# Optimization experiments

Hardware: AMD Instinct MI355X
Metric: run time of the kernel (lower is better)

The kernel has to match this reference:

```python
import jax, jax.numpy as jnp
import numpy as np

B, NE, NR, A = 512, 100000, 400, 256
ENT, REL, HIST = 200, 200, 400
ADIM = ENT + REL  # 400
HUGE = 1e31
EPS = 1e-20


def _linear(x, W, b):
    return x @ W.T + b


def setup_inputs() -> dict:
    key = jax.random.key(0)
    ks = jax.random.split(key, 26)
    w = lambda k, o, i: (jax.random.normal(k, (o, i)) * 0.02).astype(jnp.float32)
    bz = lambda o: jnp.zeros((o,), jnp.float32)
    inp = {}
    inp['H'] = jax.random.normal(ks[0], (B, HIST), jnp.float32)
    mask = (jax.random.uniform(ks[1], (B, A)) > 0.3).astype(jnp.float32)
    inp['action_mask'] = mask.at[:, 0].set(1.0)  # ensure at least one valid action
    inp['entity_emb'] = jax.random.normal(ks[2], (NE, ENT), jnp.float32) * 0.1
    inp['relation_emb'] = jax.random.normal(ks[3], (NR, REL), jnp.float32) * 0.1
    inp['W1'] = w(ks[4], ADIM, ENT + HIST + REL); inp['b1'] = bz(ADIM)
    inp['W2'] = w(ks[5], ADIM, ADIM); inp['b2'] = bz(ADIM)
    inp['W3'] = w(ks[6], REL, ENT); inp['b3'] = bz(REL)
    inp['W4'] = w(ks[7], REL, REL); inp['b4'] = bz(REL)
    inp['W5'] = w(ks[8], REL, REL + ENT); inp['b5'] = bz(REL)
    inp['W6'] = w(ks[9], REL, REL + REL); inp['b6'] = bz(REL)
    inp['Watt'] = w(ks[10], REL, ADIM + REL); inp['batt'] = bz(REL)
    inp['e'] = jax.random.randint(ks[11], (B,), 0, NE)
    inp['q'] = jax.random.randint(ks[12], (B,), 0, NR)
    inp['pred_id'] = jax.random.randint(ks[13], (B, 1), 0, NE)
    inp['r_space'] = jax.random.randint(ks[14], (B, A), 0, NR)
    inp['e_space'] = jax.random.randint(ks[15], (B, A), 0, NE)
    return inp


def reference(H, action_mask, entity_emb, relation_emb,
              W1, b1, W2, b2, W3, b3, W4, b4, W5, b5, W6, b6, Watt, batt,
              e, q, pred_id, r_space, e_space):
    # --- embed lookups ---
    Q = relation_emb[q]                 # [B, REL]
    E = entity_emb[e]                   # [B, ENT]
    # --- small MLP (dropout in eval mode -> identity) ---
    X = jax.nn.relu(_linear(jnp.concatenate([E, H, Q], -1), W1, b1))
    X2 = _linear(X, W2, b2)             # [B, ADIM]
    # --- full relation attention (multinomial sample replaced by given pred_id) ---
    pred_emb = entity_emb[pred_id]      # [B, 1, ENT]
    pred_ent_info = _linear(pred_emb, W3, b3)       # [B, 1, REL]
    relation_K = _linear(relation_emb, W4, b4)      # [NR, REL]
    local_att = jnp.einsum('bkd,rd->bkr', pred_ent_info, relation_K)  # [B,1,NR]
    beta = jnp.einsum('bkr,rd->bkd', jax.nn.softmax(local_att, -1), relation_emb).sum(1)  # [B, REL]
    # cat([R_all expand, pred_emb expand], -1).sum(1) == [sum_r R_all, NR * pred_emb]
    rel_sum = relation_emb.sum(0)                   # [REL]
    alpha_in = jnp.concatenate([jnp.broadcast_to(rel_sum, (H.shape[0], REL)),
                                NR * pred_emb[:, 0, :]], -1)
    alpha = _linear(alpha_in, W5, b5)               # [B, REL]
    V_A = _linear(jnp.concatenate([alpha, beta], -1), W6, b6)  # [B, REL]
    relation_att = jax.nn.softmax(
        _linear(jnp.concatenate([X2, V_A], -1), Watt, batt) @ relation_emb.T, -1)  # [B, NR]
    # --- policy_nn_fun: action embedding gather + masked softmax ---
    A_emb = jnp.concatenate([relation_emb[r_space], entity_emb[e_space]], -1)  # [B, A, ADIM]
    scores = jnp.einsum('bad,bd->ba', A_emb, X2) - (1.0 - action_mask) * HUGE
    action_dist = jax.nn.softmax(scores, -1)        # [B, A]
    entropy = -jnp.sum(action_dist * jnp.log(action_dist + EPS), -1)  # [B]
    return action_dist, entropy, relation_att
```

## Files before the change

### kernel.cpp

```cpp
#include <hip/hip_runtime.h>
#include <cstdint>
#include <cstddef>

#define BB 512
#define NEn 100000
#define NRr 400
#define AA 256
#define ENTd 200
#define RELd 200
#define HISTd 400
#define ADIMd 400

__device__ __forceinline__ float dot4(const float4 a, const float4 b) {
  return a.x * b.x + a.y * b.y + a.z * b.z + a.w * b.w;
}
__device__ __forceinline__ void fma4(float4& a, const float4 w, const float c) {
  a.x += w.x * c; a.y += w.y * c; a.z += w.z * c; a.w += w.w * c;
}
__device__ __forceinline__ float wave_rmax(float v) {
#pragma unroll
  for (int off = 32; off > 0; off >>= 1) v = fmaxf(v, __shfl_xor(v, off));
  return v;
}
__device__ __forceinline__ float wave_rsum(float v) {
#pragma unroll
  for (int off = 32; off > 0; off >>= 1) v += __shfl_xor(v, off);
  return v;
}

__global__ __launch_bounds__(256) void prep1_kernel(
    const float* __restrict__ rel_emb, const float* __restrict__ W4,
    const float* __restrict__ b4, const float* __restrict__ W5,
    const float* __restrict__ b5, const float* __restrict__ W6,
    const float* __restrict__ Watt, const float* __restrict__ W1,
    const float* __restrict__ W2, float* __restrict__ RK,
    float* __restrict__ P, float* __restrict__ W6bb, float* __restrict__ ab,
    float* __restrict__ relT, float* __restrict__ WaT,
    float* __restrict__ W1T, float* __restrict__ W2T) {
  int t = threadIdx.x;
  int blk = blockIdx.x;
  if (blk == 0) {
    __shared__ float rs[RELd];
    if (t < RELd) {
      float s = 0.f;
      for (int r = 0; r < NRr; r += 4) {
        s += rel_emb[(size_t)r * RELd + t] + rel_emb[(size_t)(r + 1) * RELd + t] +
             rel_emb[(size_t)(r + 2) * RELd + t] + rel_emb[(size_t)(r + 3) * RELd + t];
      }
      rs[t] = s;
    }
    __syncthreads();
    if (t < RELd) {
      float acc = b5[t];
      const float4* w = (const float4*)(W5 + (size_t)t * 400);
      const float4* rv = (const float4*)rs;
      for (int k = 0; k < 50; ++k) acc += dot4(w[k], rv[k]);
      ab[t] = acc;
    }
  } else if (blk <= 50) {
    int r0 = (blk - 1) * 8;
    __shared__ float re[8][RELd];
    for (int i = t; i < 8 * RELd; i += 256)
      re[i / RELd][i % RELd] = rel_emb[(size_t)(r0 + i / RELd) * RELd + i % RELd];
    __syncthreads();
    if (t < RELd) {
      float bv = b4[t];
      float acc[8];
#pragma unroll
      for (int s = 0; s < 8; ++s) acc[s] = bv;
      const float4* w = (const float4*)(W4 + (size_t)t * RELd);
      for (int k = 0; k < 50; ++k) {
        float4 wv = w[k];
#pragma unroll
        for (int s = 0; s < 8; ++s) acc[s] += dot4(wv, ((const float4*)re[s])[k]);
      }
#pragma unroll
      for (int s = 0; s < 8; ++s) RK[(size_t)(r0 + s) * RELd + t] = acc[s];
    }
  } else if (blk <= 75) {
    int i0 = (blk - 51) * 8;
    __shared__ float w6s[8][200];
    for (int i = t; i < 8 * 200; i += 256)
      w6s[i / 200][i % 200] = W6[(size_t)(i0 + i / 200) * 400 + i % 200];
    __syncthreads();
    if (t < 200) {
      int k = t;
      float acc[8] = {0, 0, 0, 0, 0, 0, 0, 0};
      for (int j = 0; j < 200; j += 4) {
        float r0v = W5[(size_t)j * 400 + 200 + k];
        float r1v = W5[(size_t)(j + 1) * 400 + 200 + k];
        float r2v = W5[(size_t)(j + 2) * 400 + 200 + k];
        float r3v = W5[(size_t)(j + 3) * 400 + 200 + k];
#pragma unroll
        for (int s = 0; s < 8; ++s)
          acc[s] += w6s[s][j] * r0v + w6s[s][j + 1] * r1v + w6s[s][j + 2] * r2v +
                    w6s[s][j + 3] * r3v;
      }
#pragma unroll
      for (int s = 0; s < 8; ++s) P[(size_t)(i0 + s) * 200 + k] = 400.f * acc[s];
    }
  } else if (blk <= 100) {
    int u0 = (blk - 76) * 8;
    __shared__ float wbs[8][200];
    for (int i = t; i < 8 * 200; i += 256)
      wbs[i / 200][i % 200] = Watt[(size_t)(u0 + i / 200) * 600 + 400 + i % 200];
    __syncthreads();
    if (t < 200) {
      int j = t;
      float acc[8] = {0, 0, 0, 0, 0, 0, 0, 0};
      for (int i = 0; i < 200; i += 4) {
        float r0v = W6[(size_t)i * 400 + 200 + j];
        float r1v = W6[(size_t)(i + 1) * 400 + 200 + j];
        float r2v = W6[(size_t)(i + 2) * 400 + 200 + j];
        float r3v = W6[(size_t)(i + 3) * 400 + 200 + j];
#pragma unroll
        for (int s = 0; s < 8; ++s)
          acc[s] += wbs[s][i] * r0v + wbs[s][i + 1] * r1v + wbs[s][i + 2] * r2v +
                    wbs[s][i + 3] * r3v;
      }
#pragma unroll
      for (int s = 0; s < 8; ++s) W6bb[(size_t)(u0 + s) * 200 + j] = acc[s];
    }
  } else {
    __shared__ float tlds[64][65];
    int tb = blk - 101;
    const float* src;
    float* dst;
    int M, N, LD, ti, tj;
    if (tb < 28) {
      src = rel_emb; dst = relT; M = 400; N = 200; LD = 200;
      ti = tb / 4; tj = tb % 4;
    } else if (tb < 56) {
      tb -= 28;
      src = Watt; dst = WaT; M = 200; N = 400; LD = 600;
      ti = tb / 7; tj = tb % 7;
    } else if (tb < 147) {
      tb -= 56;
      src = W1; dst = W1T; M = 400; N = 800; LD = 800;
      ti = tb / 13; tj = tb % 13;
    } else {
      tb -= 147;
      src = W2; dst = W2T; M = 400; N = 400; LD = 400;
      ti = tb / 7; tj = tb % 7;
    }
    int i0 = ti * 64, j0 = tj * 64;
    for (int idx = t; idx < 4096; idx += 256) {
      int r = idx >> 6, c = idx & 63;
      int i = i0 + r, j = j0 + c;
      if (i < M && j < N) tlds[r][c] = src[(size_t)i * LD + j];
    }
    __syncthreads();
    for (int idx = t; idx < 4096; idx += 256) {
      int r = idx >> 6, c = idx & 63;
      int j = j0 + r, i = i0 + c;
      if (i < M && j < N) dst[(size_t)j * M + i] = tlds[c][r];
    }
  }
}

__global__ __launch_bounds__(1024) void prep2_x1_kernel(
    const float* __restrict__ rel_emb, const float* __restrict__ W3,
    const float* __restrict__ b3, const float* __restrict__ W6,
    const float* __restrict__ Watt, const float* __restrict__ batt,
    const float* __restrict__ b6, const float* __restrict__ RK,
    const float* __restrict__ P, const float* __restrict__ W6bb,
    const float* __restrict__ ab, float* __restrict__ S_T,
    float* __restrict__ cvec, float* __restrict__ Q_T,
    float* __restrict__ REatt, float* __restrict__ v1,
    const float* __restrict__ ent_emb, const float* __restrict__ H,
    const int* __restrict__ e_idx, const int* __restrict__ q_idx,
    const float* __restrict__ W1T, const float* __restrict__ b1,
    float* __restrict__ X) {
  int t = threadIdx.x;
  int blk = blockIdx.x;
  if (blk < 50) {
    int r0 = blk * 8;
    __shared__ float rks[8][200];
    __shared__ float b3s[200];
    for (int i = t; i < 1600; i += 1024)
      rks[i / 200][i % 200] = RK[(size_t)r0 * 200 + i];
    if (t < 200) b3s[t] = b3[t];
    __syncthreads();
    if (t < 200) {
      int i = t;
      float acc[8] = {0, 0, 0, 0, 0, 0, 0, 0};
      for (int j = 0; j < 200; j += 4) {
        float w0 = W3[(size_t)j * 200 + i];
        float w1 = W3[(size_t)(j + 1) * 200 + i];
        float w2 = W3[(size_t)(j + 2) * 200 + i];
        float w3v = W3[(size_t)(j + 3) * 200 + i];
#pragma unroll
        for (int s = 0; s < 8; ++s)
          acc[s] += w0 * rks[s][j] + w1 * rks[s][j + 1] + w2 * rks[s][j + 2] +
                    w3v * rks[s][j + 3];
      }
      float4 s0 = make_float4(acc[0], acc[1], acc[2], acc[3]);
      float4 s1 = make_float4(acc[4], acc[5], acc[6], acc[7]);
      *(float4*)(S_T + (size_t)i * 400 + r0) = s0;
      *(float4*)(S_T + (size_t)i * 400 + r0 + 4) = s1;
    }
    if (t < 256) {
      int w = t >> 6, lane = t & 63;
      float p0 = 0.f, p1 = 0.f;
      for (int j = lane; j < 200; j += 64) {
        p0 += b3s[j] * rks[w][j];
        p1 += b3s[j] * rks[w + 4][j];
      }
      p0 = wave_rsum(p0);
      p1 = wave_rsum(p1);
      if (lane == 0) {
        cvec[r0 + w] = p0;
        cvec[r0 + w + 4] = p1;
      }
    }
  } else if (blk < 75) {
    int u0 = (blk - 50) * 8;
    __shared__ float wbs[8][200];
    for (int i = t; i < 1600; i += 1024)
      wbs[i / 200][i % 200] = Watt[(size_t)(u0 + i / 200) * 600 + 400 + i % 200];
    __syncthreads();
    if (t < 200) {
      int k = t;
      float acc[8] = {0, 0, 0, 0, 0, 0, 0, 0};
      for (int i = 0; i < 200; i += 4) {
        float r0v = P[(size_t)i * 200 + k];
        float r1v = P[(size_t)(i + 1) * 200 + k];
        float r2v = P[(size_t)(i + 2) * 200 + k];
        float r3v = P[(size_t)(i + 3) * 200 + k];
#pragma unroll
        for (int s = 0; s < 8; ++s)
          acc[s] += wbs[s][i] * r0v + wbs[s][i + 1] * r1v + wbs[s][i + 2] * r2v +
                    wbs[s][i + 3] * r3v;
      }
      float4 s0 = make_float4(acc[0], acc[1], acc[2], acc[3]);
      float4 s1 = make_float4(acc[4], acc[5], acc[6], acc[7]);
      *(float4*)(Q_T + (size_t)k * 200 + u0) = s0;
      *(float4*)(Q_T + (size_t)k * 200 + u0 + 4) = s1;
    }
  } else if (blk < 125) {
    int r0 = (blk - 75) * 8;
    __shared__ float rels[8][200];
    for (int i = t; i < 1600; i += 1024)
      rels[i / 200][i % 200] = rel_emb[(size_t)r0 * 200 + i];
    __syncthreads();
    if (t < 200) {
      float acc[8] = {0, 0, 0, 0, 0, 0, 0, 0};
      const float4* w = (const float4*)(W6bb + (size_t)t * 200);
      for (int k = 0; k < 50; ++k) {
        float4 wv = w[k];
#pragma unroll
        for (int s = 0; s < 8; ++s) acc[s] += dot4(wv, ((const float4*)rels[s])[k]);
      }
#pragma unroll
      for (int s = 0; s < 8; ++s) REatt[(size_t)(r0 + s) * 200 + t] = acc[s];
    }
  } else if (blk == 125) {
    __shared__ float abs_[200];
    __shared__ float us[200];
    if (t < 200) abs_[t] = ab[t];
    __syncthreads();
    if (t < 200) {
      float u = b6[t];
      const float4* w = (const float4*)(W6 + (size_t)t * 400);
      const float4* rv = (const float4*)abs_;
      for (int k = 0; k < 50; ++k) u += dot4(w[k], rv[k]);
      us[t] = u;
    }
    __syncthreads();
    if (t < 200) {
      float v = batt[t];
      const float4* w = (const float4*)(Watt + (size_t)t * 600 + 400);
      const float4* rv = (const float4*)us;
      for (int k = 0; k < 50; ++k) v += dot4(w[k], rv[k]);
      v1[t] = v;
    }
  } else {
    int b0 = (blk - 126) * 4;
    __shared__ float cv[4][800];
    __shared__ float prt[12800];
    for (int i = t; i < 3200; i += 1024) {
      int s = i / 800, k = i % 800;
      float v;
      if (k < ENTd)
        v = ent_emb[(size_t)e_idx[b0 + s] * ENTd + k];
      else if (k < ENTd + HISTd)
        v = H[(size_t)(b0 + s) * HISTd + (k - ENTd)];
      else
        v = rel_emb[(size_t)q_idx[b0 + s] * RELd + (k - ENTd - HISTd)];
      cv[s][k] = v;
    }
    __syncthreads();
    if (t < 800) {
      int g = t % 100, h = t / 100;
      float4 acc[4];
#pragma unroll
      for (int s = 0; s < 4; ++s) acc[s] = make_float4(0, 0, 0, 0);
      const float4* wp = ((const float4*)W1T) + g;
      int k0 = h * 100;
#pragma unroll 4
      for (int kk = 0; kk < 100; ++kk) {
        int k = k0 + kk;
        float4 wv = wp[(size_t)k * 100];
#pragma unroll
        for (int s = 0; s < 4; ++s) fma4(acc[s], wv, cv[s][k]);
      }
#pragma unroll
      for (int s = 0; s < 4; ++s)
        ((float4*)prt)[(h * 4 + s) * 100 + g] = acc[s];
    }
    __syncthreads();
    for (int i = t; i < 1600; i += 1024) {
      int s = i / 400, j = i % 400;
      float a = b1[j];
#pragma unroll
      for (int h = 0; h < 8; ++h) a += prt[(h * 4 + s) * 400 + j];
      X[(size_t)(b0 + s) * ADIMd + j] = fmaxf(a, 0.f);
    }
  }
}

__global__ __launch_bounds__(1024) void x2rx_kernel(
    const float* __restrict__ X, const float* __restrict__ W2T,
    const float* __restrict__ b2, const float* __restrict__ relT,
    float* __restrict__ X2, float* __restrict__ RX) {
  int b0 = blockIdx.x * 2;
  int t = threadIdx.x;
  __shared__ float cv[2][400];
  __shared__ float prt[6400];
  __shared__ float x2lo[2][200];
  for (int i = t; i < 800; i += 1024) cv[i / 400][i % 400] = X[(size_t)b0 * 400 + i];
  __syncthreads();
  if (t < 800) {
    int g = t % 100, h = t / 100;
    float4 accA = make_float4(0, 0, 0, 0);
    float4 accB = make_float4(0, 0, 0, 0);
    const float4* wp = ((const float4*)W2T) + g;
    int k0 = h * 50;
#pragma unroll 4
    for (int kk = 0; kk < 50; ++kk) {
      int k = k0 + kk;
      float4 wv = wp[(size_t)k * 100];
      fma4(accA, wv, cv[0][k]);
      fma4(accB, wv, cv[1][k]);
    }
    ((float4*)prt)[(h * 2 + 0) * 100 + g] = accA;
    ((float4*)prt)[(h * 2 + 1) * 100 + g] = accB;
  }
  __syncthreads();
  if (t < 800) {
    int s = t / 400, j = t % 400;
    float a = b2[j];
#pragma unroll
    for (int h = 0; h < 8; ++h) a += prt[(h * 2 + s) * 400 + j];
    X2[(size_t)(b0 + s) * ADIMd + j] = a;
    if (j < 200) x2lo[s][j] = a;
  }
  __syncthreads();
  if (t < 800) {
    int g = t % 100, h = t / 100;
    float4 accA = make_float4(0, 0, 0, 0);
    float4 accB = make_float4(0, 0, 0, 0);
    const float4* rp = ((const float4*)relT) + g;
    int k0 = h * 25;
#pragma unroll 4
    for (int kk = 0; kk < 25; ++kk) {
      int k = k0 + kk;
      float4 wv = rp[(size_t)k * 100];
      fma4(accA, wv, x2lo[0][k]);
      fma4(accB, wv, x2lo[1][k]);
    }
    ((float4*)prt)[(h * 2 + 0) * 100 + g] = accA;
    ((float4*)prt)[(h * 2 + 1) * 100 + g] = accB;
  }
  __syncthreads();
  if (t < 800) {
    int s = t / 400, r = t % 400;
    float a = 0.f;
#pragma unroll
    for (int h = 0; h < 8; ++h) a += prt[(h * 2 + s) * 400 + r];
    RX[(size_t)(b0 + s) * NRr + r] = a;
  }
}

__global__ __launch_bounds__(1024) void tail_kernel(
    const float* __restrict__ ent_emb, const int* __restrict__ pred_id,
    const float* __restrict__ X2, const float* __restrict__ S_T,
    const float* __restrict__ cvec, const float* __restrict__ Q_T,
    const float* __restrict__ REatt, const float* __restrict__ relT,
    const float* __restrict__ WaT, const float* __restrict__ v1c,
    const float* __restrict__ RX, const int* __restrict__ r_space,
    const int* __restrict__ e_space, const float* __restrict__ mask,
    float* __restrict__ out_ratt, float* __restrict__ out_dist,
    float* __restrict__ out_ent) {
  int t = threadIdx.x;
  int w = t >> 6, lane = t & 63;
  __shared__ float pes[4][200];
  __shared__ float x2s[4][400];
  __shared__ float pp[4][400];
  __shared__ float av[4][200];
  __shared__ float prt[12800];
  __shared__ float wred[4][4];
  __shared__ float x2hi[200];
  __shared__ float scl[256];
  __shared__ float wr[4];

  if (blockIdx.x < 128) {
    int b0 = blockIdx.x * 4;
    for (int i = t; i < 2400; i += 1024) {
      if (i < 800)
        pes[i / 200][i % 200] =
            ent_emb[(size_t)pred_id[b0 + i / 200] * ENTd + i % 200];
      else {
        int k = i - 800;
        x2s[k / 400][k % 400] = X2[(size_t)b0 * 400 + k];
      }
    }
    __syncthreads();
    if (t < 800) {
      int g = t % 100, h = t / 100;
      float4 acc[4];
#pragma unroll
      for (int s = 0; s < 4; ++s) acc[s] = make_float4(0, 0, 0, 0);
      const float4* sp = ((const float4*)S_T) + g;
      int k0 = h * 25;
#pragma unroll 5
      for (int kk = 0; kk < 25; ++kk) {
        int k = k0 + kk;
        float4 wv = sp[(size_t)k * 100];
#pragma unroll
        for (int s = 0; s < 4; ++s) fma4(acc[s], wv, pes[s][k]);
      }
#pragma unroll
      for (int s = 0; s < 4; ++s)
        ((float4*)prt)[(h * 4 + s) * 100 + g] = acc[s];
    }
    __syncthreads();
    for (int i = t; i < 1600; i += 1024) {
      int s = i / 400, r = i % 400;
      float a = cvec[r];
#pragma unroll
      for (int h = 0; h < 8; ++h) a += prt[(h * 4 + s) * 400 + r];
      pp[s][r] = a;
    }
    __syncthreads();
    int row = w >> 2, q = w & 3;
    {
      float m = -INFINITY;
      for (int r = q * 64 + lane; r < 400; r += 256) m = fmaxf(m, pp[row][r]);
      m = wave_rmax(m);
      if (lane == 0) wred[row][q] = m;
      __syncthreads();
      float gm = fmaxf(fmaxf(wred[row][0], wred[row][1]),
                       fmaxf(wred[row][2], wred[row][3]));
      __syncthreads();
      float sum = 0.f;
      for (int r = q * 64 + lane; r < 400; r += 256) {
        float e = expf(pp[row][r] - gm);
        pp[row][r] = e;
        sum += e;
      }
      sum = wave_rsum(sum);
      if (lane == 0) wred[row][q] = sum;
      __syncthreads();
      float inv =
          1.f / (wred[row][0] + wred[row][1] + wred[row][2] + wred[row][3]);
      for (int r = q * 64 + lane; r < 400; r += 256) pp[row][r] *= inv;
    }
    __syncthreads();
    if (t < 800) {
      int g = t % 50, h = t / 50;
      float4 acc[4];
      if (h == 0) {
        float4 v = ((const float4*)v1c)[g];
#pragma unroll
        for (int s = 0; s < 4; ++s) acc[s] = v;
      } else {
#pragma unroll
        for (int s = 0; s < 4; ++s) acc[s] = make_float4(0, 0, 0, 0);
      }
      {
        const float4* wp = ((const float4*)WaT) + g;
        int k0 = h * 25;
#pragma unroll 5
        for (int kk = 0; kk < 25; ++kk) {
          int k = k0 + kk;
          float4 wv = wp[(size_t)k * 50];
#pragma unroll
          for (int s = 0; s < 4; ++s) fma4(acc[s], wv, x2s[s][k]);
        }
      }
      if (h < 8) {
        const float4* qp = ((const float4*)Q_T) + g;
        int k0 = h * 25;
#pragma unroll 5
        for (int kk = 0; kk < 25; ++kk) {
          int k = k0 + kk;
          float4 wv = qp[(size_t)k * 50];
#pragma unroll
          for (int s = 0; s < 4; ++s) fma4(acc[s], wv, pes[s][k]);
        }
      }
      {
        const float4* rp = ((const float4*)REatt) + g;
        int r0 = h * 25;
#pragma unroll 5
        for (int kk = 0; kk < 25; ++kk) {
          int r = r0 + kk;
          float4 wv = rp[(size_t)r * 50];
#pragma unroll
          for (int s = 0; s < 4; ++s) fma4(acc[s], wv, pp[s][r]);
        }
      }
#pragma unroll
      for (int s = 0; s < 4; ++s)
        ((float4*)prt)[(h * 4 + s) * 50 + g] = acc[s];
    }
    __syncthreads();
    if (t < 800) {
      int s = t / 200, j = t % 200;
      float a = 0.f;
#pragma unroll
      for (int h = 0; h < 16; ++h) a += prt[(h * 4 + s) * 200 + j];
      av[s][j] = a;
    }
    __syncthreads();
    if (t < 800) {
      int g = t % 100, h = t / 100;
      float4 acc[4];
#pragma unroll
      for (int s = 0; s < 4; ++s) acc[s] = make_float4(0, 0, 0, 0);
      const float4* rp = ((const float4*)relT) + g;
      int k0 = h * 25;
#pragma unroll 5
      for (int kk = 0; kk < 25; ++kk) {
        int k = k0 + kk;
        float4 wv = rp[(size_t)k * 100];
#pragma unroll
        for (int s = 0; s < 4; ++s) fma4(acc[s], wv, av[s][k]);
      }
#pragma unroll
      for (int s = 0; s < 4; ++s)
        ((float4*)prt)[(h * 4 + s) * 100 + g] = acc[s];
    }
    __syncthreads();
    for (int i = t; i < 1600; i += 1024) {
      int s = i / 400, r = i % 400;
      float a = 0.f;
#pragma unroll
      for (int h = 0; h < 8; ++h) a += prt[(h * 4 + s) * 400 + r];
      pp[s][r] = a;
    }
    __syncthreads();
    {
      float m = -INFINITY;
      for (int r = q * 64 + lane; r < 400; r += 256) m = fmaxf(m, pp[row][r]);
      m = wave_rmax(m);
      if (lane == 0) wred[row][q] = m;
      __syncthreads();
      float gm = fmaxf(fmaxf(wred[row][0], wred[row][1]),
                       fmaxf(wred[row][2], wred[row][3]));
      __syncthreads();
      float sum = 0.f;
      for (int r = q * 64 + lane; r < 400; r += 256) {
        float e = expf(pp[row][r] - gm);
        pp[row][r] = e;
        sum += e;
      }
      sum = wave_rsum(sum);
      if (lane == 0) wred[row][q] = sum;
      __syncthreads();
      float inv =
          1.f / (wred[row][0] + wred[row][1] + wred[row][2] + wred[row][3]);
      for (int r = q * 64 + lane; r < 400; r += 256)
        out_ratt[(size_t)(b0 + row) * 400 + r] = pp[row][r] * inv;
    }
  } else {
    int b = blockIdx.x - 128;
    if (t >= 200 && t < 400) x2hi[t - 200] = X2[(size_t)b * ADIMd + t];
    __syncthreads();
    const float4* xh = (const float4*)x2hi;
    {
      int abase = w * 16;
      int ei[16];
#pragma unroll
      for (int u = 0; u < 16; ++u) ei[u] = e_space[(size_t)b * AA + abase + u];
      float p[16];
      if (lane < 50) {
        float4 xv = xh[lane];
#pragma unroll
        for (int u = 0; u < 16; ++u) {
          float4 vv = ((const float4*)(ent_emb + (size_t)ei[u] * ENTd))[lane];
          p[u] = dot4(vv, xv);
        }
      } else {
#pragma unroll
        for (int u = 0; u < 16; ++u) p[u] = 0.f;
      }
#pragma unroll
      for (int off = 32; off > 0; off >>= 1) {
#pragma unroll
        for (int u = 0; u < 16; ++u) p[u] += __shfl_xor(p[u], off);
      }
      if (lane == 0) {
#pragma unroll
        for (int u = 0; u < 16; ++u) scl[abase + u] = p[u];
      }
    }
    __syncthreads();
    float sc = -INFINITY;
    if (t < 256) {
      int r = r_space[(size_t)b * AA + t];
      sc = scl[t] + RX[(size_t)b * NRr + r] -
           (1.f - mask[(size_t)b * AA + t]) * 1e31f;
    }
    __syncthreads();
    if (w < 4) {
      float m = wave_rmax(sc);
      if (lane == 0) wr[w] = m;
    }
    __syncthreads();
    float gm = fmaxf(fmaxf(wr[0], wr[1]), fmaxf(wr[2], wr[3]));
    float e = (t < 256) ? expf(sc - gm) : 0.f;
    __syncthreads();
    if (w < 4) {
      float s2 = wave_rsum(e);
      if (lane == 0) wr[w] = s2;
    }
    __syncthreads();
    float gs = wr[0] + wr[1] + wr[2] + wr[3];
    float p = e / gs;
    if (t < 256) out_dist[(size_t)b * AA + t] = p;
    float ent = (t < 256) ? -p * logf(p + 1e-20f) : 0.f;
    __syncthreads();
    if (w < 4) {
      float s3 = wave_rsum(ent);
      if (lane == 0) wr[w] = s3;
    }
    __syncthreads();
    if (t == 0) out_ent[b] = wr[0] + wr[1] + wr[2] + wr[3];
  }
}

extern "C" void kernel_launch(void* const* d_in, const int* in_sizes, int n_in,
                              void* d_out, int out_size, void* d_ws,
                              size_t ws_size, hipStream_t stream) {
  const float* H = (const float*)d_in[0];
  const float* mask = (const float*)d_in[1];
  const float* ent_emb = (const float*)d_in[2];
  const float* rel_emb = (const float*)d_in[3];
  const float* W1 = (const float*)d_in[4];
  const float* b1 = (const float*)d_in[5];
  const float* W2 = (const float*)d_in[6];
  const float* b2 = (const float*)d_in[7];
  const float* W3 = (const float*)d_in[8];
  const float* b3 = (const float*)d_in[9];
  const float* W4 = (const float*)d_in[10];
  const float* b4 = (const float*)d_in[11];
  const float* W5 = (const float*)d_in[12];
  const float* b5 = (const float*)d_in[13];
  const float* W6 = (const float*)d_in[14];
  const float* b6 = (const float*)d_in[15];
  const float* Watt = (const float*)d_in[16];
  const float* batt = (const float*)d_in[17];
  const int* e_idx = (const int*)d_in[18];
  const int* q_idx = (const int*)d_in[19];
  const int* pred_id = (const int*)d_in[20];
  const int* r_space = (const int*)d_in[21];
  const int* e_space = (const int*)d_in[22];

  float* ws = (float*)d_ws;
  float* RK = ws;
  float* S_T = ws + 80000;
  float* cvec = ws + 160000;
  float* P = ws + 160512;
  float* Q_T = ws + 200512;
  float* W6bb = ws + 240512;
  float* REatt = ws + 280512;
  float* relT = ws + 360512;
  float* WaT = ws + 440512;
  float* W1T = ws + 520512;
  float* W2T = ws + 840512;
  float* ab = ws + 1000512;
  float* v1 = ws + 1000768;
  float* X = ws + 1001024;
  float* X2 = ws + 1205824;
  float* RX = ws + 1410624;

  float* out = (float*)d_out;
  float* out_dist = out;
  float* out_ent = out + BB * AA;
  float* out_ratt = out + BB * AA + BB;

  hipLaunchKernelGGL(prep1_kernel, dim3(297), dim3(256), 0, stream, rel_emb,
                     W4, b4, W5, b5, W6, Watt, W1, W2, RK, P, W6bb, ab, relT,
                     WaT, W1T, W2T);
  hipLaunchKernelGGL(prep2_x1_kernel, dim3(254), dim3(1024), 0, stream,
                     rel_emb, W3, b3, W6, Watt, batt, b6, RK, P, W6bb, ab,
                     S_T, cvec, Q_T, REatt, v1, ent_emb, H, e_idx, q_idx,
                     W1T, b1, X);
  hipLaunchKernelGGL(x2rx_kernel, dim3(256), dim3(1024), 0, stream, X, W2T,
                     b2, relT, X2, RX);
  hipLaunchKernelGGL(tail_kernel, dim3(640), dim3(1024), 0, stream, ent_emb,
                     pred_id, X2, S_T, cvec, Q_T, REatt, relT, WaT, v1, RX,
                     r_space, e_space, mask, out_ratt, out_dist, out_ent);
}
```

Baseline: 99.18 us.

## Fuse action scoring and masked softmax into X2 kernel, split relation-attention tail

Moves the per-row action embedding gather, score computation, masked softmax and entropy from the tail kernel into the X2/RX kernel. RX now stays in shared memory instead of round-tripping through global memory, and each block handles two batch rows. The remaining tail kernel computes only the relation attention and is launched with 128 blocks instead of 640 heterogeneous ones. This removes a global intermediate and rebalances the work, but it lengthens the X2 kernel and its serial chain of synchronizations.

```diff
diff --git a/kernel.cpp b/kernel.cpp
--- a/kernel.cpp
+++ b/kernel.cpp
@@ -319,15 +319,22 @@
   }
 }
 
-__global__ __launch_bounds__(1024) void x2rx_kernel(
+__global__ __launch_bounds__(1024) void x2rx_scores_kernel(
     const float* __restrict__ X, const float* __restrict__ W2T,
     const float* __restrict__ b2, const float* __restrict__ relT,
-    float* __restrict__ X2, float* __restrict__ RX) {
+    const float* __restrict__ ent_emb, const int* __restrict__ r_space,
+    const int* __restrict__ e_space, const float* __restrict__ mask,
+    float* __restrict__ X2, float* __restrict__ out_dist,
+    float* __restrict__ out_ent) {
   int b0 = blockIdx.x * 2;
   int t = threadIdx.x;
+  int w = t >> 6, lane = t & 63;
   __shared__ float cv[2][400];
   __shared__ float prt[6400];
-  __shared__ float x2lo[2][200];
+  __shared__ float x2full[2][400];
+  __shared__ float rxl[2][400];
+  __shared__ float scl[512];
+  __shared__ float wred2[2][4];
   for (int i = t; i < 800; i += 1024) cv[i / 400][i % 400] = X[(size_t)b0 * 400 + i];
   __syncthreads();
   if (t < 800) {
@@ -353,7 +360,7 @@
 #pragma unroll
     for (int h = 0; h < 8; ++h) a += prt[(h * 2 + s) * 400 + j];
     X2[(size_t)(b0 + s) * ADIMd + j] = a;
-    if (j < 200) x2lo[s][j] = a;
+    x2full[s][j] = a;
   }
   __syncthreads();
   if (t < 800) {
@@ -362,12 +369,12 @@
     float4 accB = make_float4(0, 0, 0, 0);
     const float4* rp = ((const float4*)relT) + g;
     int k0 = h * 25;
-#pragma unroll 4
+#pragma unroll 5
     for (int kk = 0; kk < 25; ++kk) {
       int k = k0 + kk;
       float4 wv = rp[(size_t)k * 100];
-      fma4(accA, wv, x2lo[0][k]);
-      fma4(accB, wv, x2lo[1][k]);
+      fma4(accA, wv, x2full[0][k]);
+      fma4(accB, wv, x2full[1][k]);
     }
     ((float4*)prt)[(h * 2 + 0) * 100 + g] = accA;
     ((float4*)prt)[(h * 2 + 1) * 100 + g] = accB;
@@ -378,20 +385,94 @@
     float a = 0.f;
 #pragma unroll
     for (int h = 0; h < 8; ++h) a += prt[(h * 2 + s) * 400 + r];
-    RX[(size_t)(b0 + s) * NRr + r] = a;
-  }
-}
-
-__global__ __launch_bounds__(1024) void tail_kernel(
+    rxl[s][r] = a;
+  }
+  __syncthreads();
+  {
+    int s = w >> 3;
+    int wa = (w & 7) * 32;
+    const float4* xh = ((const float4*)x2full[s]) + 50;
+    for (int c = 0; c < 2; ++c) {
+      int abase = wa + c * 16;
+      int ei[16];
+#pragma unroll
+      for (int u = 0; u < 16; ++u)
+        ei[u] = e_space[(size_t)(b0 + s) * AA + abase + u];
+      float p[16];
+      if (lane < 50) {
+        float4 xv = xh[lane];
+#pragma unroll
+        for (int u = 0; u < 16; ++u) {
+          float4 vv = ((const float4*)(ent_emb + (size_t)ei[u] * ENTd))[lane];
+          p[u] = dot4(vv, xv);
+        }
+      } else {
+#pragma unroll
+        for (int u = 0; u < 16; ++u) p[u] = 0.f;
+      }
+#pragma unroll
+      for (int off = 32; off > 0; off >>= 1) {
+#pragma unroll
+        for (int u = 0; u < 16; ++u) p[u] += __shfl_xor(p[u], off);
+      }
+      if (lane == 0) {
+#pragma unroll
+        for (int u = 0; u < 16; ++u) scl[s * 256 + abase + u] = p[u];
+      }
+    }
+  }
+  __syncthreads();
+  float sc = -INFINITY;
+  if (t < 512) {
+    int s = t / 256, a = t % 256;
+    int r = r_space[(size_t)(b0 + s) * AA + a];
+    sc = scl[t] + rxl[s][r] - (1.f - mask[(size_t)(b0 + s) * AA + a]) * 1e31f;
+  }
+  if (w < 8) {
+    float m = wave_rmax(sc);
+    if (lane == 0) wred2[w >> 2][w & 3] = m;
+  }
+  __syncthreads();
+  float e = 0.f;
+  if (t < 512) {
+    int s = t / 256;
+    float gm = fmaxf(fmaxf(wred2[s][0], wred2[s][1]),
+                     fmaxf(wred2[s][2], wred2[s][3]));
+    e = expf(sc - gm);
+  }
+  __syncthreads();
+  if (w < 8) {
+    float s2 = wave_rsum(e);
+    if (lane == 0) wred2[w >> 2][w & 3] = s2;
+  }
+  __syncthreads();
+  float p = 0.f;
+  if (t < 512) {
+    int s = t / 256;
+    float gs = wred2[s][0] + wred2[s][1] + wred2[s][2] + wred2[s][3];
+    p = e / gs;
+    out_dist[(size_t)(b0 + s) * AA + (t % 256)] = p;
+  }
+  float ent = (t < 512) ? -p * logf(p + 1e-20f) : 0.f;
+  __syncthreads();
+  if (w < 8) {
+    float s3 = wave_rsum(ent);
+    if (lane == 0) wred2[w >> 2][w & 3] = s3;
+  }
+  __syncthreads();
+  if (t == 0)
+    out_ent[b0] = wred2[0][0] + wred2[0][1] + wred2[0][2] + wred2[0][3];
+  if (t == 1)
+    out_ent[b0 + 1] = wred2[1][0] + wred2[1][1] + wred2[1][2] + wred2[1][3];
+}
+
+__global__ __launch_bounds__(1024) void fused_mid_kernel(
     const float* __restrict__ ent_emb, const int* __restrict__ pred_id,
     const float* __restrict__ X2, const float* __restrict__ S_T,
     const float* __restrict__ cvec, const float* __restrict__ Q_T,
     const float* __restrict__ REatt, const float* __restrict__ relT,
     const float* __restrict__ WaT, const float* __restrict__ v1c,
-    const float* __restrict__ RX, const int* __restrict__ r_space,
-    const int* __restrict__ e_space, const float* __restrict__ mask,
-    float* __restrict__ out_ratt, float* __restrict__ out_dist,
-    float* __restrict__ out_ent) {
+    float* __restrict__ out_ratt) {
   int t = threadIdx.x;
   int w = t >> 6, lane = t & 63;
   __shared__ float pes[4][200];
@@ -400,244 +481,174 @@
   __shared__ float av[4][200];
   __shared__ float prt[12800];
   __shared__ float wred[4][4];
-  __shared__ float x2hi[200];
-  __shared__ float scl[256];
-  __shared__ float wr[4];
-
-  if (blockIdx.x < 128) {
-    int b0 = blockIdx.x * 4;
-    for (int i = t; i < 2400; i += 1024) {
-      if (i < 800)
-        pes[i / 200][i % 200] =
-            ent_emb[(size_t)pred_id[b0 + i / 200] * ENTd + i % 200];
-      else {
-        int k = i - 800;
-        x2s[k / 400][k % 400] = X2[(size_t)b0 * 400 + k];
-      }
-    }
-    __syncthreads();
-    if (t < 800) {
-      int g = t % 100, h = t / 100;
-      float4 acc[4];
+  int b0 = blockIdx.x * 4;
+  for (int i = t; i < 2400; i += 1024) {
+    if (i < 800)
+      pes[i / 200][i % 200] =
+          ent_emb[(size_t)pred_id[b0 + i / 200] * ENTd + i % 200];
+    else {
+      int k = i - 800;
+      x2s[k / 400][k % 400] = X2[(size_t)b0 * 400 + k];
+    }
+  }
+  __syncthreads();
+  if (t < 800) {
+    int g = t % 100, h = t / 100;
+    float4 acc[4];
+#pragma unroll
+    for (int s = 0; s < 4; ++s) acc[s] = make_float4(0, 0, 0, 0);
+    const float4* sp = ((const float4*)S_T) + g;
+    int k0 = h * 25;
+#pragma unroll 5
+    for (int kk = 0; kk < 25; ++kk) {
+      int k = k0 + kk;
+      float4 wv = sp[(size_t)k * 100];
+#pragma unroll
+      for (int s = 0; s < 4; ++s) fma4(acc[s], wv, pes[s][k]);
+    }
+#pragma unroll
+    for (int s = 0; s < 4; ++s)
+      ((float4*)prt)[(h * 4 + s) * 100 + g] = acc[s];
+  }
+  __syncthreads();
+  for (int i = t; i < 1600; i += 1024) {
+    int s = i / 400, r = i % 400;
+    float a = cvec[r];
+#pragma unroll
+    for (int h = 0; h < 8; ++h) a += prt[(h * 4 + s) * 400 + r];
+    pp[s][r] = a;
+  }
+  __syncthreads();
+  int row = w >> 2, q = w & 3;
+  {
+    float m = -INFINITY;
+    for (int r = q * 64 + lane; r < 400; r += 256) m = fmaxf(m, pp[row][r]);
+    m = wave_rmax(m);
+    if (lane == 0) wred[row][q] = m;
+    __syncthreads();
+    float gm = fmaxf(fmaxf(wred[row][0], wred[row][1]),
+                     fmaxf(wred[row][2], wred[row][3]));
+    __syncthreads();
+    float sum = 0.f;
+    for (int r = q * 64 + lane; r < 400; r += 256) {
+      float e = expf(pp[row][r] - gm);
+      pp[row][r] = e;
+      sum += e;
+    }
+    sum = wave_rsum(sum);
+    if (lane == 0) wred[row][q] = sum;
+    __syncthreads();
+    float inv =
+        1.f / (wred[row][0] + wred[row][1] + wred[row][2] + wred[row][3]);
+    for (int r = q * 64 + lane; r < 400; r += 256) pp[row][r] *= inv;
+  }
+  __syncthreads();
+  if (t < 800) {
+    int g = t % 50, h = t / 50;
+    float4 acc[4];
+    if (h == 0) {
+      float4 v = ((const float4*)v1c)[g];
+#pragma unroll
+      for (int s = 0; s < 4; ++s) acc[s] = v;
+    } else {
 #pragma unroll
       for (int s = 0; s < 4; ++s) acc[s] = make_float4(0, 0, 0, 0);
-      const float4* sp = ((const float4*)S_T) + g;
+    }
+    {
+      const float4* wp = ((const float4*)WaT) + g;
       int k0 = h * 25;
 #pragma unroll 5
       for (int kk = 0; kk < 25; ++kk) {
         int k = k0 + kk;
-        float4 wv = sp[(size_t)k * 100];
-#pragma unroll
-        for (int s = 0; s < 4; ++s) fma4(acc[s], wv, pes[s][k]);
-      }
-#pragma unroll
-      for (int s = 0; s < 4; ++s)
-        ((float4*)prt)[(h * 4 + s) * 100 + g] = acc[s];
-    }
-    __syncthreads();
-    for (int i = t; i < 1600; i += 1024) {
-      int s = i / 400, r = i % 400;
-      float a = cvec[r];
-#pragma unroll
-      for (int h = 0; h < 8; ++h) a += prt[(h * 4 + s) * 400 + r];
-      pp[s][r] = a;
-    }
-    __syncthreads();
-    int row = w >> 2, q = w & 3;
-    {
-      float m = -INFINITY;
-      for (int r = q * 64 + lane; r < 400; r += 256) m = fmaxf(m, pp[row][r]);
-      m = wave_rmax(m);
-      if (lane == 0) wred[row][q] = m;
-      __syncthreads();
-      float gm = fmaxf(fmaxf(wred[row][0], wred[row][1]),
-                       fmaxf(wred[row][2], wred[row][3]));
-      __syncthreads();
-      float sum = 0.f;
-      for (int r = q * 64 + lane; r < 400; r += 256) {
-        float e = expf(pp[row][r] - gm);
-        pp[row][r] = e;
-        sum += e;
-      }
-      sum = wave_rsum(sum);
-      if (lane == 0) wred[row][q] = sum;
-      __syncthreads();
-      float inv =
-          1.f / (wred[row][0] + wred[row][1] + wred[row][2] + wred[row][3]);
-      for (int r = q * 64 + lane; r < 400; r += 256) pp[row][r] *= inv;
-    }
-    __syncthreads();
-    if (t < 800) {
-      int g = t % 50, h = t / 50;
-      float4 acc[4];
-      if (h == 0) {
-        float4 v = ((const float4*)v1c)[g];
-#pragma unroll
-        for (int s = 0; s < 4; ++s) acc[s] = v;
-      } else {
-#pragma unroll
-        for (int s = 0; s < 4; ++s) acc[s] = make_float4(0, 0, 0, 0);
-      }
-      {
-        const float4* wp = ((const float4*)WaT) + g;
-        int k0 = h * 25;
-#pragma unroll 5
-        for (int kk = 0; kk < 25; ++kk) {
-          int k = k0 + kk;
-          float4 wv = wp[(size_t)k * 50];
-#pragma unroll
-          for (int s = 0; s < 4; ++s) fma4(acc[s], wv, x2s[s][k]);
-        }
-      }
-      if (h < 8) {
-        const float4* qp = ((const float4*)Q_T) + g;
-        int k0 = h * 25;
-#pragma unroll 5
-        for (int kk = 0; kk < 25; ++kk) {
-          int k = k0 + kk;
-          float4 wv = qp[(size_t)k * 50];
-#pragma unroll
-          for (int s = 0; s < 4; ++s) fma4(acc[s], wv, pes[s][k]);
-        }
-      }
-      {
-        const float4* rp = ((const float4*)REatt) + g;
-        int r0 = h * 25;
-#pragma unroll 5
-        for (int kk = 0; kk < 25; ++kk) {
-          int r = r0 + kk;
-          float4 wv = rp[(size_t)r * 50];
-#pragma unroll
-          for (int s = 0; s < 4; ++s) fma4(acc[s], wv, pp[s][r]);
-        }
-      }
-#pragma unroll
-      for (int s = 0; s < 4; ++s)
-        ((float4*)prt)[(h * 4 + s) * 50 + g] = acc[s];
-    }
-    __syncthreads();
-    if (t < 800) {
-      int s = t / 200, j = t % 200;
-      float a = 0.f;
-#pragma unroll
-      for (int h = 0; h < 16; ++h) a += prt[(h * 4 + s) * 200 + j];
-      av[s][j] = a;
-    }
-    __syncthreads();
-    if (t < 800) {
-      int g = t % 100, h = t / 100;
-      float4 acc[4];
-#pragma unroll
-      for (int s = 0; s < 4; ++s) acc[s] = make_float4(0, 0, 0, 0);
-      const float4* rp = ((const float4*)relT) + g;
+        float4 wv = wp[(size_t)k * 50];
+#pragma unroll
+        for (int s = 0; s < 4; ++s) fma4(acc[s], wv, x2s[s][k]);
+      }
+    }
+    if (h < 8) {
+      const float4* qp = ((const float4*)Q_T) + g;
       int k0 = h * 25;
 #pragma unroll 5
       for (int kk = 0; kk < 25; ++kk) {
         int k = k0 + kk;
-        float4 wv = rp[(size_t)k * 100];
-#pragma unroll
-        for (int s = 0; s < 4; ++s) fma4(acc[s], wv, av[s][k]);
-      }
-#pragma unroll
-      for (int s = 0; s < 4; ++s)
-        ((float4*)prt)[(h * 4 + s) * 100 + g] = acc[s];
-    }
-    __syncthreads();
-    for (int i = t; i < 1600; i += 1024) {
-      int s = i / 400, r = i % 400;
-      float a = 0.f;
-#pragma unroll
-      for (int h = 0; h < 8; ++h) a += prt[(h * 4 + s) * 400 + r];
-      pp[s][r] = a;
-    }
-    __syncthreads();
+        float4 wv = qp[(size_t)k * 50];
+#pragma unroll
+        for (int s = 0; s < 4; ++s) fma4(acc[s], wv, pes[s][k]);
+      }
+    }
     {
-      float m = -INFINITY;
-      for (int r = q * 64 + lane; r < 400; r += 256) m = fmaxf(m, pp[row][r]);
-      m = wave_rmax(m);
-      if (lane == 0) wred[row][q] = m;
-      __syncthreads();
-      float gm = fmaxf(fmaxf(wred[row][0], wred[row][1]),
-                       fmaxf(wred[row][2], wred[row][3]));
-      __syncthreads();
-      float sum = 0.f;
-      for (int r = q * 64 + lane; r < 400; r += 256) {
-        float e = expf(pp[row][r] - gm);
-        pp[row][r] = e;
-        sum += e;
-      }
-      sum = wave_rsum(sum);
-      if (lane == 0) wred[row][q] = sum;
-      __syncthreads();
-      float inv =
-          1.f / (wred[row][0] + wred[row][1] + wred[row][2] + wred[row][3]);
-      for (int r = q * 64 + lane; r < 400; r += 256)
-        out_ratt[(size_t)(b0 + row) * 400 + r] = pp[row][r] * inv;
-    }
-  } else {
-    int b = blockIdx.x - 128;
-    if (t >= 200 && t < 400) x2hi[t - 200] = X2[(size_t)b * ADIMd + t];
-    __syncthreads();
-    const float4* xh = (const float4*)x2hi;
-    {
-      int abase = w * 16;
-      int ei[16];
-#pragma unroll
-      for (int u = 0; u < 16; ++u) ei[u] = e_space[(size_t)b * AA + abase + u];
-      float p[16];
-      if (lane < 50) {
-        float4 xv = xh[lane];
-#pragma unroll
-        for (int u = 0; u < 16; ++u) {
-          float4 vv = ((const float4*)(ent_emb + (size_t)ei[u] * ENTd))[lane];
-          p[u] = dot4(vv, xv);
-        }
-      } else {
-#pragma unroll
-        for (int u = 0; u < 16; ++u) p[u] = 0.f;
-      }
-#pragma unroll
-      for (int off = 32; off > 0; off >>= 1) {
-#pragma unroll
-        for (int u = 0; u < 16; ++u) p[u] += __shfl_xor(p[u], off);
-      }
-      if (lane == 0) {
-#pragma unroll
-        for (int u = 0; u < 16; ++u) scl[abase + u] = p[u];
-      }
-    }
-    __syncthreads();
-    float sc = -INFINITY;
-    if (t < 256) {
-      int r = r_space[(size_t)b * AA + t];
-      sc = scl[t] + RX[(size_t)b * NRr + r] -
-           (1.f - mask[(size_t)b * AA + t]) * 1e31f;
-    }
-    __syncthreads();
-    if (w < 4) {
-      float m = wave_rmax(sc);
-      if (lane == 0) wr[w] = m;
-    }
-    __syncthreads();
-    float gm = fmaxf(fmaxf(wr[0], wr[1]), fmaxf(wr[2], wr[3]));
-    float e = (t < 256) ? expf(sc - gm) : 0.f;
-    __syncthreads();
-    if (w < 4) {
-      float s2 = wave_rsum(e);
-      if (lane == 0) wr[w] = s2;
-    }
-    __syncthreads();
-    float gs = wr[0] + wr[1] + wr[2] + wr[3];
-    float p = e / gs;
-    if (t < 256) out_dist[(size_t)b * AA + t] = p;
-    float ent = (t < 256) ? -p * logf(p + 1e-20f) : 0.f;
-    __syncthreads();
-    if (w < 4) {
-      float s3 = wave_rsum(ent);
-      if (lane == 0) wr[w] = s3;
-    }
-    __syncthreads();
-    if (t == 0) out_ent[b] = wr[0] + wr[1] + wr[2] + wr[3];
+      const float4* rp = ((const float4*)REatt) + g;
+      int r0 = h * 25;
+#pragma unroll 5
+      for (int kk = 0; kk < 25; ++kk) {
+        int r = r0 + kk;
+        float4 wv = rp[(size_t)r * 50];
+#pragma unroll
+        for (int s = 0; s < 4; ++s) fma4(acc[s], wv, pp[s][r]);
+      }
+    }
+#pragma unroll
+    for (int s = 0; s < 4; ++s)
+      ((float4*)prt)[(h * 4 + s) * 50 + g] = acc[s];
+  }
+  __syncthreads();
+  if (t < 800) {
+    int s = t / 200, j = t % 200;
+    float a = 0.f;
+#pragma unroll
+    for (int h = 0; h < 16; ++h) a += prt[(h * 4 + s) * 200 + j];
+    av[s][j] = a;
+  }
+  __syncthreads();
+  if (t < 800) {
+    int g = t % 100, h = t / 100;
+    float4 acc[4];
+#pragma unroll
+    for (int s = 0; s < 4; ++s) acc[s] = make_float4(0, 0, 0, 0);
+    const float4* rp = ((const float4*)relT) + g;
+    int k0 = h * 25;
+#pragma unroll 5
+    for (int kk = 0; kk < 25; ++kk) {
+      int k = k0 + kk;
+      float4 wv = rp[(size_t)k * 100];
+#pragma unroll
+      for (int s = 0; s < 4; ++s) fma4(acc[s], wv, av[s][k]);
+    }
+#pragma unroll
+    for (int s = 0; s < 4; ++s)
+      ((float4*)prt)[(h * 4 + s) * 100 + g] = acc[s];
+  }
+  __syncthreads();
+  for (int i = t; i < 1600; i += 1024) {
+    int s = i / 400, r = i % 400;
+    float a = 0.f;
+#pragma unroll
+    for (int h = 0; h < 8; ++h) a += prt[(h * 4 + s) * 400 + r];
+    pp[s][r] = a;
+  }
+  __syncthreads();
+  {
+    float m = -INFINITY;
+    for (int r = q * 64 + lane; r < 400; r += 256) m = fmaxf(m, pp[row][r]);
+    m = wave_rmax(m);
+    if (lane == 0) wred[row][q] = m;
+    __syncthreads();
+    float gm = fmaxf(fmaxf(wred[row][0], wred[row][1]),
+                     fmaxf(wred[row][2], wred[row][3]));
+    __syncthreads();
+    float sum = 0.f;
+    for (int r = q * 64 + lane; r < 400; r += 256) {
+      float e = expf(pp[row][r] - gm);
+      pp[row][r] = e;
+      sum += e;
+    }
+    sum = wave_rsum(sum);
+    if (lane == 0) wred[row][q] = sum;
+    __syncthreads();
+    float inv =
+        1.f / (wred[row][0] + wred[row][1] + wred[row][2] + wred[row][3]);
+    for (int r = q * 64 + lane; r < 400; r += 256)
+      out_ratt[(size_t)(b0 + row) * 400 + r] = pp[row][r] * inv;
   }
 }
 
@@ -684,7 +695,6 @@
   float* v1 = ws + 1000768;
   float* X = ws + 1001024;
   float* X2 = ws + 1205824;
-  float* RX = ws + 1410624;
 
   float* out = (float*)d_out;
   float* out_dist = out;
@@ -698,9 +708,10 @@
                      rel_emb, W3, b3, W6, Watt, batt, b6, RK, P, W6bb, ab,
                      S_T, cvec, Q_T, REatt, v1, ent_emb, H, e_idx, q_idx,
                      W1T, b1, X);
-  hipLaunchKernelGGL(x2rx_kernel, dim3(256), dim3(1024), 0, stream, X, W2T,
-                     b2, relT, X2, RX);
-  hipLaunchKernelGGL(tail_kernel, dim3(640), dim3(1024), 0, stream, ent_emb,
-                     pred_id, X2, S_T, cvec, Q_T, REatt, relT, WaT, v1, RX,
-                     r_space, e_space, mask, out_ratt, out_dist, out_ent);
-}
+  hipLaunchKernelGGL(x2rx_scores_kernel, dim3(256), dim3(1024), 0, stream, X,
+                     W2T, b2, relT, ent_emb, r_space, e_space, mask, X2,
+                     out_dist, out_ent);
+  hipLaunchKernelGGL(fused_mid_kernel, dim3(128), dim3(1024), 0, stream,
+                     ent_emb, pred_id, X2, S_T, cvec, Q_T, REatt, relT, WaT,
+                     v1, out_ratt);
+}
```

New measurement: 118.8 us. +19.8%, slower.
